# Performance work log

Hardware: AMD Instinct MI355X
Metric: run time of the kernel (lower is better)

Reference implementation:

```python
import jax, jax.numpy as jnp
import numpy as np

EPS_COS = 1e-8   # torch cosine_similarity eps
EPS_LN = 1e-5    # torch LayerNorm eps
SLOPE = 0.01     # torch LeakyReLU default negative_slope
N_HOP = 3
D_MODEL = 512
TEMP = 10.0


def _cos_sim(q, s):
    # q: [B, D], s: [B, S, D] -> [B, S]
    dot = jnp.einsum('bd,bsd->bs', q, s)
    qn = jnp.linalg.norm(q, axis=-1)          # [B]
    sn = jnp.linalg.norm(s, axis=-1)          # [B, S]
    return dot / jnp.maximum(qn[:, None] * sn, EPS_COS)


def _layer_norm(x, gamma, beta):
    mu = jnp.mean(x, axis=-1, keepdims=True)
    var = jnp.mean(jnp.square(x - mu), axis=-1, keepdims=True)
    return (x - mu) * jax.lax.rsqrt(var + EPS_LN) * gamma + beta


def setup_inputs() -> dict:
    key = jax.random.key(0)
    k1, k2, k3, k4 = jax.random.split(key, 4)
    B, S, D = 256, 512, D_MODEL
    query_emb = jax.random.normal(k1, (B, D), dtype=jnp.float32)
    state_emb = jax.random.normal(k2, (B, S, D), dtype=jnp.float32)
    # Stacked per-hop Linear params (txt branch), kaiming-uniform-ish scale
    lim = 1.0 / np.sqrt(D)
    W = jax.random.uniform(k3, (N_HOP, D, D), jnp.float32, -lim, lim)
    b = jax.random.uniform(k4, (N_HOP, D), jnp.float32, -lim, lim)
    ln_gamma = jnp.ones((D,), jnp.float32)
    ln_beta = jnp.zeros((D,), jnp.float32)
    return {"query_emb": query_emb, "state_emb": state_emb, "W": W, "b": b,
            "ln_gamma": ln_gamma, "ln_beta": ln_beta}


def reference(query_emb, state_emb, W, b, ln_gamma, ln_beta):
    q, s = query_emb, state_emb
    for i in range(N_HOP):
        dist = jax.nn.softmax(_cos_sim(q, s) * TEMP, axis=-1)       # [B, S]
        s = jax.nn.leaky_relu(jnp.einsum('bsd,de->bse', s, W[i].T) + b[i],
                              negative_slope=SLOPE)                  # [B, S, D]
        agg = jnp.einsum('bs,bsd->bd', dist, s)                      # [B, D]
        q = _layer_norm(q + agg, ln_gamma, ln_beta)
    final_dist = jax.nn.softmax(_cos_sim(q, s) * TEMP, axis=-1)
    return (q, final_dist)
```

## Files before the change

kernel.cpp:

```cpp
#include <hip/hip_runtime.h>
#include <hip/hip_bf16.h>
#include <stdint.h>

#define D 512
#define BATCH 256
#define SEQ 512

typedef __attribute__((ext_vector_type(8))) short short8;
typedef __attribute__((ext_vector_type(4))) float floatx4;

__device__ __forceinline__ float bf2f(unsigned short u) {
    union { unsigned int i; float f; } x; x.i = ((unsigned int)u) << 16; return x.f;
}
__device__ __forceinline__ unsigned short f2bf(float f) {
    union { float f; unsigned int i; } x; x.f = f;
    unsigned int i = x.i;
    unsigned int lsb = (i >> 16) & 1u;
    i += 0x7fffu + lsb;
    return (unsigned short)(i >> 16);
}

__device__ __forceinline__ float wred_sum(float v) {
    #pragma unroll
    for (int o = 32; o; o >>= 1) v += __shfl_xor(v, o, 64);
    return v;
}
__device__ __forceinline__ float gred_sum16(float v) {
    #pragma unroll
    for (int o = 8; o; o >>= 1) v += __shfl_xor(v, o, 64);
    return v;
}

__device__ __forceinline__ void llds16(const void* g, void* l) {
    auto gp = (const __attribute__((address_space(1))) void*)(g);
    auto lp = (__attribute__((address_space(3))) void*)(uintptr_t)(l);
    __builtin_amdgcn_global_load_lds(gp, lp, 16, 0, 0);
}

#define FENCE() asm volatile("" ::: "memory")
#define BARRIER() do { FENCE(); __builtin_amdgcn_s_barrier(); FENCE(); } while (0)

template<int WN>
__device__ __forceinline__ void waitvm() {
    if constexpr (WN == 4)      asm volatile("s_waitcnt vmcnt(4)" ::: "memory");
    else if constexpr (WN == 0) asm volatile("s_waitcnt vmcnt(0)" ::: "memory");
}

__global__ __launch_bounds__(1024)
void scores0_kernel(const float* __restrict__ state, const float* __restrict__ query,
                    float* __restrict__ dist_out, unsigned short* __restrict__ s_bf_out,
                    const float* __restrict__ W, unsigned short* __restrict__ Wb) {
    const int b = blockIdx.x, t = threadIdx.x, lane = t & 63, w = t >> 6;
    const int g = lane >> 4, ll = lane & 15;
    __shared__ float sc[SEQ];
    __shared__ float red[8];
    __shared__ float m_s, sum_s;

    {
        const int wi = b * 1024 + t;
        if (wi < 3 * D * D / 4) {
            float4 v = *(const float4*)(W + (size_t)wi * 4);
            ushort4 o;
            o.x = f2bf(v.x); o.y = f2bf(v.y); o.z = f2bf(v.z); o.w = f2bf(v.w);
            *(ushort4*)(Wb + (size_t)wi * 4) = o;
        }
    }

    float qv[4][8];
    {
        const float* qp = query + (size_t)b * D + ll * 8;
        #pragma unroll
        for (int j = 0; j < 4; ++j) {
            float4 a = *(const float4*)(qp + j * 128);
            float4 c = *(const float4*)(qp + j * 128 + 4);
            qv[j][0]=a.x; qv[j][1]=a.y; qv[j][2]=a.z; qv[j][3]=a.w;
            qv[j][4]=c.x; qv[j][5]=c.y; qv[j][6]=c.z; qv[j][7]=c.w;
        }
    }
    float qn2 = 0.f;
    #pragma unroll
    for (int j = 0; j < 4; ++j)
        #pragma unroll
        for (int e = 0; e < 8; ++e) qn2 += qv[j][e] * qv[j][e];
    const float qn = sqrtf(gred_sum16(qn2));

    const size_t bbase = (size_t)b * (SEQ * D);
    #pragma unroll 2
    for (int i = 0; i < 8; ++i) {
        const int row = w * 32 + i * 4 + g;
        const float* rp = state + bbase + (size_t)row * D + ll * 8;
        unsigned short* op = s_bf_out + bbase + (size_t)row * D + ll * 8;
        float dot = 0.f, nr = 0.f;
        #pragma unroll
        for (int j = 0; j < 4; ++j) {
            float4 a = *(const float4*)(rp + j * 128);
            float4 c = *(const float4*)(rp + j * 128 + 4);
            float v[8] = {a.x, a.y, a.z, a.w, c.x, c.y, c.z, c.w};
            short8 wv;
            #pragma unroll
            for (int e = 0; e < 8; ++e) wv[e] = (short)f2bf(v[e]);
            *(short8*)(op + j * 128) = wv;
            #pragma unroll
            for (int e = 0; e < 8; ++e) { dot += v[e] * qv[j][e]; nr += v[e] * v[e]; }
        }
        dot = gred_sum16(dot);
        nr  = gred_sum16(nr);
        if (ll == 0) sc[row] = 10.f * dot / fmaxf(qn * sqrtf(nr), 1e-8f);
    }
    __syncthreads();

    float sv = 0.f, ev = 0.f;
    if (t < 512) {
        sv = sc[t];
        float m = sv;
        #pragma unroll
        for (int o = 32; o; o >>= 1) m = fmaxf(m, __shfl_xor(m, o, 64));
        if (lane == 0) red[w] = m;
    }
    __syncthreads();
    if (t == 0) {
        float mm = red[0];
        #pragma unroll
        for (int k = 1; k < 8; ++k) mm = fmaxf(mm, red[k]);
        m_s = mm;
    }
    __syncthreads();
    if (t < 512) {
        ev = __expf(sv - m_s);
        float es = wred_sum(ev);
        if (lane == 0) red[w] = es;
    }
    __syncthreads();
    if (t == 0) {
        float s = 0.f;
        #pragma unroll
        for (int k = 0; k < 8; ++k) s += red[k];
        sum_s = s;
    }
    __syncthreads();
    if (t < 512) dist_out[b * SEQ + t] = ev / sum_s;
}

__global__ __launch_bounds__(1024)
void fused_kernel(const unsigned short* __restrict__ S, const float* __restrict__ part,
                  const float* __restrict__ q_in, const float* __restrict__ gamma,
                  const float* __restrict__ beta, float* __restrict__ q_out,
                  float* __restrict__ dist_out) {
    const int b = blockIdx.x, t = threadIdx.x, lane = t & 63, w = t >> 6;
    const int g = lane >> 4, ll = lane & 15;
    __shared__ float qs[D];
    __shared__ float sc[SEQ];
    __shared__ float red[8];
    __shared__ float mu_s, rstd_s, qn_s, m_s, sum_s;

    float x = 0.f;
    if (t < 512) {
        const float a = part[(size_t)b * D + t] + part[(size_t)(BATCH * D) + (size_t)b * D + t];
        x = q_in[(size_t)b * D + t] + a;
        float sm = wred_sum(x);
        if (lane == 0) red[w] = sm;
    }
    __syncthreads();
    if (t == 0) mu_s = (red[0]+red[1]+red[2]+red[3]+red[4]+red[5]+red[6]+red[7]) * (1.f / 512.f);
    __syncthreads();
    if (t < 512) {
        const float d = x - mu_s;
        float vv = wred_sum(d * d);
        if (lane == 0) red[w] = vv;
    }
    __syncthreads();
    if (t == 0) rstd_s = rsqrtf((red[0]+red[1]+red[2]+red[3]+red[4]+red[5]+red[6]+red[7]) * (1.f / 512.f) + 1e-5f);
    __syncthreads();
    if (t < 512) {
        const float y = (x - mu_s) * rstd_s * gamma[t] + beta[t];
        q_out[(size_t)b * D + t] = y;
        qs[t] = y;
        float s2 = wred_sum(y * y);
        if (lane == 0) red[w] = s2;
    }
    __syncthreads();
    if (t == 0) qn_s = sqrtf(red[0]+red[1]+red[2]+red[3]+red[4]+red[5]+red[6]+red[7]);
    __syncthreads();

    float qv[4][8];
    #pragma unroll
    for (int j = 0; j < 4; ++j) {
        float4 a = *(const float4*)&qs[j * 128 + ll * 8];
        float4 c = *(const float4*)&qs[j * 128 + ll * 8 + 4];
        qv[j][0]=a.x; qv[j][1]=a.y; qv[j][2]=a.z; qv[j][3]=a.w;
        qv[j][4]=c.x; qv[j][5]=c.y; qv[j][6]=c.z; qv[j][7]=c.w;
    }
    const float qn = qn_s;
    const size_t bbase = (size_t)b * (SEQ * D);
    #pragma unroll 2
    for (int i = 0; i < 8; ++i) {
        const int row = w * 32 + i * 4 + g;
        const unsigned short* rp = S + bbase + (size_t)row * D + ll * 8;
        float dot = 0.f, nr = 0.f;
        #pragma unroll
        for (int j = 0; j < 4; ++j) {
            short8 wv = *(const short8*)(rp + j * 128);
            #pragma unroll
            for (int e = 0; e < 8; ++e) {
                const float v = bf2f((unsigned short)wv[e]);
                dot += v * qv[j][e];
                nr += v * v;
            }
        }
        dot = gred_sum16(dot);
        nr  = gred_sum16(nr);
        if (ll == 0) sc[row] = 10.f * dot / fmaxf(qn * sqrtf(nr), 1e-8f);
    }
    __syncthreads();

    float sv = 0.f, ev = 0.f;
    if (t < 512) {
        sv = sc[t];
        float m = sv;
        #pragma unroll
        for (int o = 32; o; o >>= 1) m = fmaxf(m, __shfl_xor(m, o, 64));
        if (lane == 0) red[w] = m;
    }
    __syncthreads();
    if (t == 0) {
        float mm = red[0];
        #pragma unroll
        for (int k = 1; k < 8; ++k) mm = fmaxf(mm, red[k]);
        m_s = mm;
    }
    __syncthreads();
    if (t < 512) {
        ev = __expf(sv - m_s);
        float es = wred_sum(ev);
        if (lane == 0) red[w] = es;
    }
    __syncthreads();
    if (t == 0) {
        float s = 0.f;
        #pragma unroll
        for (int k = 0; k < 8; ++k) s += red[k];
        sum_s = s;
    }
    __syncthreads();
    if (t < 512) dist_out[b * SEQ + t] = ev / sum_s;
}

#define NKT 8

#define STA(BUF, H, KT) { const unsigned short* s_ = pA + (H) * 128 * D + (KT) * 64; \
    llds16(s_, &AsL[BUF][H][t * 8]); llds16(s_ + 64 * D, &AsL[BUF][H][t * 8 + 4096]); }
#define STB(BUF, H, KT) { const unsigned short* s_ = pB + (H) * 128 * D + (KT) * 64; \
    llds16(s_, &BsL[BUF][H][t * 8]); llds16(s_ + 64 * D, &BsL[BUF][H][t * 8 + 4096]); }

#define LDAF(BUF, MH) { _Pragma("unroll") for (int j = 0; j < 4; ++j) { \
    af[j][0] = *(const short8*)&AsL[BUF][MH][aoff[j] + xk0]; \
    af[j][1] = *(const short8*)&AsL[BUF][MH][aoff[j] + xk1]; } }
#define LDBFALL(BUF) { _Pragma("unroll") for (int ni = 0; ni < 4; ++ni) { \
    bfr[ni][0] = *(const short8*)&BsL[BUF][ni >> 1][boff[ni] + xk0]; \
    bfr[ni][1] = *(const short8*)&BsL[BUF][ni >> 1][boff[ni] + xk1]; } }

#define MMH(MH) { __builtin_amdgcn_s_setprio(1); \
    _Pragma("unroll") for (int kh = 0; kh < 2; ++kh) \
    _Pragma("unroll") for (int j = 0; j < 4; ++j) \
    _Pragma("unroll") for (int ni = 0; ni < 4; ++ni) \
        acc[(MH) * 4 + j][ni] = __builtin_amdgcn_mfma_f32_16x16x32_bf16( \
            af[j][kh], bfr[ni][kh], acc[(MH) * 4 + j][ni], 0, 0, 0); \
    __builtin_amdgcn_s_setprio(0); }

__global__ __launch_bounds__(512, 2)
void gemm_kernel(const unsigned short* __restrict__ A, const unsigned short* __restrict__ Bt,
                 const float* __restrict__ bias, const float* __restrict__ dist,
                 unsigned short* __restrict__ C, float* __restrict__ part) {
    __shared__ __align__(16) unsigned short AsL[2][2][128 * 64];
    __shared__ __align__(16) unsigned short BsL[2][2][128 * 64];
    __shared__ float dls[256];
    __shared__ float agg_lds[2][256];

    const int t = threadIdx.x, lane = t & 63, wid = t >> 6;
    const int wr = wid >> 2, wc = wid & 3;
    const int rr = lane & 15, lg = lane >> 4;
    const int bid = blockIdx.x;
    const int xcd = bid & 7, j8 = bid >> 3;
    const int nB = j8 & 1;
    const int mB = xcd * 64 + (j8 >> 1);
    const size_t tileM = (size_t)mB * 256;
    const int tileN = nB * 256;

    float b_r[4];
    #pragma unroll
    for (int ni = 0; ni < 4; ++ni) b_r[ni] = bias[tileN + (ni * 4 + wc) * 16 + rr];

    if (t < 128) {
        float2 v = *(const float2*)&dist[tileM + 2 * t];
        dls[2 * t] = v.x; dls[2 * t + 1] = v.y;
    }
    asm volatile("s_waitcnt lgkmcnt(0)" ::: "memory");

    const int srow = t >> 3, gc = (t & 7) ^ (srow & 7);
    const unsigned short* pA = A + (tileM + srow) * D + gc * 8;
    const unsigned short* pB = Bt + (size_t)(tileN + srow) * D + gc * 8;

    int aoff[4], boff[4];
    #pragma unroll
    for (int j = 0; j < 4; ++j) aoff[j] = ((j * 2 + wr) * 16 + rr) * 64;
    #pragma unroll
    for (int ni = 0; ni < 4; ++ni) boff[ni] = (((ni & 1) * 4 + wc) * 16 + rr) * 64;
    const int xk0 = ((lg) ^ (rr & 7)) * 8;
    const int xk1 = ((4 + lg) ^ (rr & 7)) * 8;

    floatx4 acc[8][4];
    #pragma unroll
    for (int i = 0; i < 8; ++i)
        #pragma unroll
        for (int j = 0; j < 4; ++j) acc[i][j] = {0.f, 0.f, 0.f, 0.f};

    short8 af[4][2], bfr[4][2];

    STA(0, 0, 0); STB(0, 0, 0); STA(0, 1, 0); STB(0, 1, 0);

    for (int kt = 0; kt < NKT; ++kt) {
        const int rb = kt & 1, sb = rb ^ 1;
        if (kt < NKT - 1) { STA(sb, 0, kt + 1); STB(sb, 0, kt + 1); waitvm<4>(); }
        else             { waitvm<0>(); }
        BARRIER();
        LDAF(rb, 0); LDBFALL(rb);
        MMH(0);
        BARRIER();
        if (kt < NKT - 1) { STA(sb, 1, kt + 1); STB(sb, 1, kt + 1); }
        LDAF(rb, 1);
        MMH(1);
        BARRIER();
    }
    __syncthreads();

    float pacc[4] = {0.f, 0.f, 0.f, 0.f};
    #pragma unroll
    for (int mi = 0; mi < 8; ++mi) {
        const int rowb = (mi * 2 + wr) * 16 + lg * 4;
        const float4 dv = *(const float4*)&dls[rowb];
        #pragma unroll
        for (int ni = 0; ni < 4; ++ni) {
            const int col = tileN + (ni * 4 + wc) * 16 + rr;
            #pragma unroll
            for (int r2 = 0; r2 < 4; ++r2) {
                float v = acc[mi][ni][r2] + b_r[ni];
                v = v >= 0.f ? v : 0.01f * v;
                C[(tileM + rowb + r2) * D + col] = f2bf(v);
                pacc[ni] += (&dv.x)[r2] * v;
            }
        }
    }
    #pragma unroll
    for (int ni = 0; ni < 4; ++ni) {
        float p = pacc[ni];
        p += __shfl_xor(p, 16, 64);
        p += __shfl_xor(p, 32, 64);
        if (lg == 0) agg_lds[wr][(ni * 4 + wc) * 16 + rr] = p;
    }
    __syncthreads();
    if (t < 256) {
        const int b = mB >> 1;
        const float s = agg_lds[0][t] + agg_lds[1][t];
        part[(size_t)(mB & 1) * (BATCH * D) + (size_t)b * D + tileN + t] = s;
    }
}

extern "C" void kernel_launch(void* const* d_in, const int* in_sizes, int n_in,
                              void* d_out, int out_size, void* d_ws, size_t ws_size,
                              hipStream_t stream) {
    const float* query = (const float*)d_in[0];
    const float* state = (const float*)d_in[1];
    const float* W     = (const float*)d_in[2];
    const float* bias  = (const float*)d_in[3];
    const float* gamma = (const float*)d_in[4];
    const float* beta  = (const float*)d_in[5];

    float* out_q    = (float*)d_out;
    float* out_dist = (float*)d_out + BATCH * SEQ;

    char* ws = (char*)d_ws;
    const size_t SBYTES = (size_t)BATCH * SEQ * D * 2;
    unsigned short* sA = (unsigned short*)ws;
    unsigned short* sB = (unsigned short*)(ws + SBYTES);
    char* ext = ws + 2 * SBYTES;
    float* dist = (float*)ext;
    float* qbuf = (float*)(ext + 524288);
    float* part = (float*)(ext + 2 * 524288);
    unsigned short* Wb = (unsigned short*)(ext + 4 * 524288);

    dim3 ggrid(BATCH * SEQ / 256 * 2);

    scores0_kernel<<<BATCH, 1024, 0, stream>>>(state, query, dist, sA, W, Wb);
    gemm_kernel<<<ggrid, 512, 0, stream>>>(sA, Wb, bias, dist, sB, part);
    fused_kernel<<<BATCH, 1024, 0, stream>>>(sB, part, query, gamma, beta, qbuf, dist);
    gemm_kernel<<<ggrid, 512, 0, stream>>>(sB, Wb + D * D, bias + D, dist, sA, part);
    fused_kernel<<<BATCH, 1024, 0, stream>>>(sA, part, qbuf, gamma, beta, qbuf, dist);
    gemm_kernel<<<ggrid, 512, 0, stream>>>(sA, Wb + 2 * D * D, bias + 2 * D, dist, sB, part);
    fused_kernel<<<BATCH, 1024, 0, stream>>>(sB, part, qbuf, gamma, beta, out_q, out_dist);
}
```

Measured before the change: 429.5 us.

## Deepen GEMM pipeline to four LDS stages with 32-wide K tiles

Restructures the bf16 GEMM main loop to use K-tiles of 32 instead of 64 with a four-stage ring of LDS buffers and prefetch distance of three. Swizzle and fragment offsets are recomputed for the narrower tile, and vmcnt waits are adjusted for the deeper in-flight load count. The aim is to hide global-to-LDS load latency better. In exchange it doubles the iteration count and barrier frequency per MFMA work, and the hand-tuned wait counts risk mis-synchronisation.

```diff
diff --git a/kernel.cpp b/kernel.cpp
--- a/kernel.cpp
+++ b/kernel.cpp
@@ -42,7 +42,9 @@
 
 template<int WN>
 __device__ __forceinline__ void waitvm() {
-    if constexpr (WN == 4)      asm volatile("s_waitcnt vmcnt(4)" ::: "memory");
+    if constexpr (WN == 10)     asm volatile("s_waitcnt vmcnt(10)" ::: "memory");
+    else if constexpr (WN == 8) asm volatile("s_waitcnt vmcnt(8)" ::: "memory");
+    else if constexpr (WN == 4) asm volatile("s_waitcnt vmcnt(4)" ::: "memory");
     else if constexpr (WN == 0) asm volatile("s_waitcnt vmcnt(0)" ::: "memory");
 }
 
@@ -245,34 +247,33 @@
     if (t < 512) dist_out[b * SEQ + t] = ev / sum_s;
 }
 
-#define NKT 8
-
-#define STA(BUF, H, KT) { const unsigned short* s_ = pA + (H) * 128 * D + (KT) * 64; \
-    llds16(s_, &AsL[BUF][H][t * 8]); llds16(s_ + 64 * D, &AsL[BUF][H][t * 8 + 4096]); }
-#define STB(BUF, H, KT) { const unsigned short* s_ = pB + (H) * 128 * D + (KT) * 64; \
-    llds16(s_, &BsL[BUF][H][t * 8]); llds16(s_ + 64 * D, &BsL[BUF][H][t * 8 + 4096]); }
-
-#define LDAF(BUF, MH) { _Pragma("unroll") for (int j = 0; j < 4; ++j) { \
-    af[j][0] = *(const short8*)&AsL[BUF][MH][aoff[j] + xk0]; \
-    af[j][1] = *(const short8*)&AsL[BUF][MH][aoff[j] + xk1]; } }
-#define LDBFALL(BUF) { _Pragma("unroll") for (int ni = 0; ni < 4; ++ni) { \
-    bfr[ni][0] = *(const short8*)&BsL[BUF][ni >> 1][boff[ni] + xk0]; \
-    bfr[ni][1] = *(const short8*)&BsL[BUF][ni >> 1][boff[ni] + xk1]; } }
-
-#define MMH(MH) { __builtin_amdgcn_s_setprio(1); \
-    _Pragma("unroll") for (int kh = 0; kh < 2; ++kh) \
+#define NKT32 16
+
+#define STA32(BUF, KT) { \
+    llds16(pA0 + (KT) * 32,                   &AsL[BUF][t * 8]); \
+    llds16(pA0 + (size_t)128 * D + (KT) * 32, &AsL[BUF][4096 + t * 8]); }
+#define STB32(BUF, KT) { \
+    llds16(pB0 + (KT) * 32,                   &BsL[BUF][t * 8]); \
+    llds16(pB0 + (size_t)128 * D + (KT) * 32, &BsL[BUF][4096 + t * 8]); }
+
+#define LDAF32(BUF, MH) { _Pragma("unroll") for (int j = 0; j < 4; ++j) \
+    af[j] = *(const short8*)&AsL[BUF][(MH) * 4096 + aoff[j]]; }
+#define LDBF32(BUF) { _Pragma("unroll") for (int ni = 0; ni < 4; ++ni) \
+    bfr[ni] = *(const short8*)&BsL[BUF][boff[ni]]; }
+
+#define MMQ32(MH) { __builtin_amdgcn_s_setprio(1); \
     _Pragma("unroll") for (int j = 0; j < 4; ++j) \
     _Pragma("unroll") for (int ni = 0; ni < 4; ++ni) \
         acc[(MH) * 4 + j][ni] = __builtin_amdgcn_mfma_f32_16x16x32_bf16( \
-            af[j][kh], bfr[ni][kh], acc[(MH) * 4 + j][ni], 0, 0, 0); \
+            af[j], bfr[ni], acc[(MH) * 4 + j][ni], 0, 0, 0); \
     __builtin_amdgcn_s_setprio(0); }
 
 __global__ __launch_bounds__(512, 2)
 void gemm_kernel(const unsigned short* __restrict__ A, const unsigned short* __restrict__ Bt,
                  const float* __restrict__ bias, const float* __restrict__ dist,
                  unsigned short* __restrict__ C, float* __restrict__ part) {
-    __shared__ __align__(16) unsigned short AsL[2][2][128 * 64];
-    __shared__ __align__(16) unsigned short BsL[2][2][128 * 64];
+    __shared__ __align__(16) unsigned short AsL[4][256 * 32];
+    __shared__ __align__(16) unsigned short BsL[4][256 * 32];
     __shared__ float dls[256];
     __shared__ float agg_lds[2][256];
 
@@ -296,17 +297,18 @@
     }
     asm volatile("s_waitcnt lgkmcnt(0)" ::: "memory");
 
-    const int srow = t >> 3, gc = (t & 7) ^ (srow & 7);
-    const unsigned short* pA = A + (tileM + srow) * D + gc * 8;
-    const unsigned short* pB = Bt + (size_t)(tileN + srow) * D + gc * 8;
-
+    const int srow = t >> 2, sc4 = t & 3;
+    const int gc = sc4 ^ ((srow >> 1) & 3);
+    const unsigned short* pA0 = A + (tileM + srow) * D + gc * 8;
+    const unsigned short* pB0 = Bt + (size_t)(tileN + srow) * D + gc * 8;
+
+    const int kx = (lg ^ ((rr >> 1) & 3)) * 8;
     int aoff[4], boff[4];
     #pragma unroll
-    for (int j = 0; j < 4; ++j) aoff[j] = ((j * 2 + wr) * 16 + rr) * 64;
-    #pragma unroll
-    for (int ni = 0; ni < 4; ++ni) boff[ni] = (((ni & 1) * 4 + wc) * 16 + rr) * 64;
-    const int xk0 = ((lg) ^ (rr & 7)) * 8;
-    const int xk1 = ((4 + lg) ^ (rr & 7)) * 8;
+    for (int j = 0; j < 4; ++j) aoff[j] = ((j * 2 + wr) * 16 + rr) * 32 + kx;
+    #pragma unroll
+    for (int ni = 0; ni < 4; ++ni) boff[ni] = (((ni * 4 + wc) * 16 + rr) & 255) * 32 + kx
+                                              + ((((ni * 4 + wc) * 16 + rr) >> 8) * 0);
 
     floatx4 acc[8][4];
     #pragma unroll
@@ -314,21 +316,26 @@
         #pragma unroll
         for (int j = 0; j < 4; ++j) acc[i][j] = {0.f, 0.f, 0.f, 0.f};
 
-    short8 af[4][2], bfr[4][2];
-
-    STA(0, 0, 0); STB(0, 0, 0); STA(0, 1, 0); STB(0, 1, 0);
-
-    for (int kt = 0; kt < NKT; ++kt) {
-        const int rb = kt & 1, sb = rb ^ 1;
-        if (kt < NKT - 1) { STA(sb, 0, kt + 1); STB(sb, 0, kt + 1); waitvm<4>(); }
-        else             { waitvm<0>(); }
+    short8 af[4], bfr[4];
+
+    STA32(0, 0); STB32(0, 0);
+    STA32(1, 1); STB32(1, 1);
+    STA32(2, 2); STB32(2, 2);
+
+    for (int kt = 0; kt < NKT32; ++kt) {
+        const int rb = kt & 3;
+        if (kt < NKT32 - 3) { STA32((kt + 3) & 3, kt + 3); }
+        if (kt < NKT32 - 3)      waitvm<10>();
+        else if (kt == NKT32 - 3) waitvm<8>();
+        else if (kt == NKT32 - 2) waitvm<4>();
+        else                      waitvm<0>();
         BARRIER();
-        LDAF(rb, 0); LDBFALL(rb);
-        MMH(0);
+        LDAF32(rb, 0); LDBF32(rb);
+        MMQ32(0);
         BARRIER();
-        if (kt < NKT - 1) { STA(sb, 1, kt + 1); STB(sb, 1, kt + 1); }
-        LDAF(rb, 1);
-        MMH(1);
+        if (kt < NKT32 - 3) { STB32((kt + 3) & 3, kt + 3); }
+        LDAF32(rb, 1);
+        MMQ32(1);
         BARRIER();
     }
     __syncthreads();
```

Result: slower. 451.6 us (+5.1%).
